# Kernel tuning notes

Measured on AMD Instinct MI355X. Metric: run time of the kernel, lower is better.

Reference implementation:

```python
import math
import jax, jax.numpy as jnp
import numpy as np

B, T, C = 2, 2048, 1024
H, Ca = 16, 64


def setup_inputs() -> dict:
    key = jax.random.key(0)
    ks = jax.random.split(key, 5)
    # kaiming-uniform-ish scale for weights
    wb = 1.0 / math.sqrt(C)
    return {
        "x": jax.random.normal(ks[0], (B, T, C), dtype=jnp.float32),
        "w_q": jax.random.uniform(ks[1], (H, C, Ca), jnp.float32, -wb, wb),
        "w_k": jax.random.uniform(ks[2], (H, C, Ca), jnp.float32, -wb, wb),
        "w_v": jax.random.uniform(ks[3], (H, C, Ca), jnp.float32, -wb, wb),
        "w_o": jax.random.uniform(ks[4], (C, C), jnp.float32, -wb, wb),
    }


def reference(x, w_q, w_k, w_v, w_o):
    # x: [B,T,C]; w_q/w_k/w_v: [H,C,Ca]; w_o: [C,C]
    scale = 1.0 / math.sqrt(w_q.shape[-1])
    q = jnp.einsum("btc,hca->bhta", x, w_q)  # [B,H,T,Ca]
    k = jnp.einsum("btc,hca->bhta", x, w_k)
    v = jnp.einsum("btc,hca->bhta", x, w_v)
    s = jnp.einsum("bhta,bhsa->bhts", q, k)  # [B,H,T,T]
    # faithful to original: mask where tril(s)==0, scale applied after masking
    s_hat = jnp.where(jnp.tril(s) == 0, -jnp.inf, s * scale)
    a = jax.nn.softmax(s_hat, axis=-1)
    y = jnp.einsum("bhts,bhsa->bhta", a, v)  # [B,H,T,Ca]
    y_cat = y.transpose(0, 2, 1, 3).reshape(x.shape)  # [B,T,C]
    return y_cat @ w_o
```

## Files before the change

kernel.cpp:

```cpp
#include <hip/hip_runtime.h>
#include <stdint.h>

#define Bc 2
#define Tc 2048
#define Cn 1024
#define Hc 16
#define CAc 64

typedef __attribute__((ext_vector_type(8))) short short8;
typedef __attribute__((ext_vector_type(4))) float f32x4;

#define QSCALE 0.18033688011112042f

__device__ __forceinline__ unsigned short f2bf(float f) {
    unsigned int u = __builtin_bit_cast(unsigned int, f);
    return (unsigned short)((u + 0x7fffu + ((u >> 16) & 1u)) >> 16);
}
__device__ __forceinline__ unsigned int pack_rne(float a, float b) {
    return (unsigned int)f2bf(a) | ((unsigned int)f2bf(b) << 16);
}
__device__ __forceinline__ unsigned int pack_trunc(float a, float b) {
    return __builtin_amdgcn_perm(__builtin_bit_cast(unsigned int, b),
                                 __builtin_bit_cast(unsigned int, a), 0x07060302u);
}

__device__ __forceinline__ void async_cp16(const unsigned short* g, unsigned short* l) {
    __builtin_amdgcn_global_load_lds(
        (const __attribute__((address_space(1))) unsigned int*)g,
        (__attribute__((address_space(3))) unsigned int*)l,
        16, 0, 0);
}

__device__ __forceinline__ int detect_bf16(const unsigned short* x) {
    int c = 0;
#pragma unroll
    for (int i = 0; i < 64; i++) {
        unsigned short u = x[i * 2];
        int e = (u >> 7) & 0xFF;
        c += (e >= 0x68 && e <= 0x90);
    }
    return c > 32;
}

__device__ __forceinline__ unsigned short ld_elem(const void* base, size_t off, int isbf) {
    return isbf ? ((const unsigned short*)base)[off] : f2bf(((const float*)base)[off]);
}

__global__ __launch_bounds__(256) void prep(
    const void* __restrict__ xin, unsigned short* __restrict__ xb,
    const void* __restrict__ wq, const void* __restrict__ wk,
    const void* __restrict__ wv, const void* __restrict__ wo,
    unsigned short* __restrict__ wT, unsigned short* __restrict__ woT)
{
    const int isbf = detect_bf16((const unsigned short*)xin);
    const int bx = blockIdx.x;
    if (bx < 4096) {
        if (isbf) return;
        int idx = (bx * 256 + threadIdx.x) * 4;
        const float* xf = (const float*)xin;
        float4 v = *(const float4*)(xf + idx);
        uint2 p;
        p.x = pack_rne(v.x, v.y);
        p.y = pack_rne(v.z, v.w);
        *(uint2*)(&xb[idx]) = p;
        return;
    }
    __shared__ unsigned short tile[32][33];
    const int t = threadIdx.x;
    const int tx = t & 31, ty = t >> 5;
    const void* src;
    unsigned short* dst;
    int R, Cw, r0, c0;
    if (bx < 7168) {
        int rem0 = bx - 4096;
        int g = rem0 >> 6;
        int rem = rem0 & 63;
        int ct = rem >> 1;
        int at = rem & 1;
        int proj = g >> 4, h = g & 15;
        const void* wsel = (proj == 0) ? wq : ((proj == 1) ? wk : wv);
        src = isbf ? (const void*)((const unsigned short*)wsel + (size_t)h * Cn * CAc)
                   : (const void*)((const float*)wsel + (size_t)h * Cn * CAc);
        dst = wT + (size_t)g * CAc * Cn;
        R = Cn; Cw = CAc; r0 = ct * 32; c0 = at * 32;
    } else {
        int rem = bx - 7168;
        src = wo; dst = woT;
        R = Cn; Cw = Cn;
        r0 = (rem >> 5) * 32; c0 = (rem & 31) * 32;
    }
#pragma unroll
    for (int j = 0; j < 4; j++)
        tile[ty + j * 8][tx] = ld_elem(src, (size_t)(r0 + ty + j * 8) * Cw + c0 + tx, isbf);
    __syncthreads();
#pragma unroll
    for (int j = 0; j < 4; j++)
        dst[(size_t)(c0 + ty + j * 8) * R + r0 + tx] = tile[tx][ty + j * 8];
}

__global__ __launch_bounds__(128, 2) void gemm_qkv(
    const void* __restrict__ xin,
    const unsigned short* __restrict__ xb,
    const unsigned short* __restrict__ Bt,
    unsigned short* __restrict__ o0,
    unsigned short* __restrict__ o1,
    unsigned short* __restrict__ o2)
{
    __shared__ alignas(16) unsigned short SH[4][128 * 32];
    const int tid = threadIdx.x;
    const int wave = tid >> 6, lane = tid & 63;
    const int l15 = lane & 15, quad = lane >> 4;
    const int mBase = blockIdx.y * 128, nBase = blockIdx.x * 128;
    const int mOff = wave * 64;

    const int isbf = detect_bf16((const unsigned short*)xin);
    const unsigned short* Amat = isbf ? (const unsigned short*)xin : xb;

    const int srow = lane >> 2;
    const int sgc  = (lane & 3) ^ (srow & 3);
    const int sw = (quad ^ (l15 & 3)) * 8;

    f32x4 acc[4][8];
#pragma unroll
    for (int i = 0; i < 4; i++)
#pragma unroll
        for (int j = 0; j < 8; j++)
            acc[i][j] = (f32x4){0.f, 0.f, 0.f, 0.f};

#pragma unroll
    for (int t = 0; t < 4; t++) {
        int rl = wave * 64 + t * 16;
        async_cp16(Amat + (size_t)(mBase + rl + srow) * Cn + sgc * 8, &SH[0][rl * 32]);
        async_cp16(Bt   + (size_t)(nBase + rl + srow) * Cn + sgc * 8, &SH[2][rl * 32]);
    }
    __syncthreads();

    for (int kk = 0; kk < 32; kk++) {
        const int cur = kk & 1;
        if (kk < 31) {
            const int k1 = (kk + 1) * 32;
#pragma unroll
            for (int t = 0; t < 4; t++) {
                int rl = wave * 64 + t * 16;
                async_cp16(Amat + (size_t)(mBase + rl + srow) * Cn + k1 + sgc * 8, &SH[1 - cur][rl * 32]);
                async_cp16(Bt   + (size_t)(nBase + rl + srow) * Cn + k1 + sgc * 8, &SH[3 - cur][rl * 32]);
            }
        }
        short8 af[4], bfr[8];
#pragma unroll
        for (int i = 0; i < 4; i++)
            af[i] = *(const short8*)(&SH[cur][(mOff + i * 16 + l15) * 32 + sw]);
#pragma unroll
        for (int j = 0; j < 8; j++)
            bfr[j] = *(const short8*)(&SH[2 + cur][(j * 16 + l15) * 32 + sw]);
#pragma unroll
        for (int i = 0; i < 4; i++)
#pragma unroll
            for (int j = 0; j < 8; j++)
                acc[i][j] = __builtin_amdgcn_mfma_f32_16x16x32_bf16(af[i], bfr[j], acc[i][j], 0, 0, 0);
        __syncthreads();
    }

    const int bb = mBase >> 11;
    if (nBase < 2048) {
        const float sc = (nBase < 1024) ? QSCALE : 1.0f;
        unsigned short* dst = (nBase < 1024) ? o0 : o1;
#pragma unroll
        for (int i = 0; i < 4; i++) {
            int m0 = mBase + mOff + i * 16 + quad * 4;
            int t0 = m0 & (Tc - 1);
#pragma unroll
            for (int j = 0; j < 8; j++) {
                int n = nBase + j * 16 + l15;
                int h = (n >> 6) & 15, a = n & 63;
                size_t base = ((size_t)(bb * Hc + h) * Tc + t0) * CAc + a;
#pragma unroll
                for (int r = 0; r < 4; r++)
                    dst[base + (size_t)r * CAc] = f2bf(acc[i][j][r] * sc);
            }
        }
    } else {
        unsigned short* Cl = &SH[0][0];
#pragma unroll
        for (int i = 0; i < 4; i++) {
            int c16 = wave * 8 + i * 2 + (quad >> 1);
            int p = quad & 1;
#pragma unroll
            for (int j = 0; j < 8; j++) {
                int nl = j * 16 + l15;
                int cs = c16 ^ (nl & 7);
                uint2 v8;
                v8.x = pack_rne(acc[i][j][0], acc[i][j][1]);
                v8.y = pack_rne(acc[i][j][2], acc[i][j][3]);
                *(uint2*)(&Cl[nl * 128 + cs * 8 + p * 4]) = v8;
            }
        }
        __syncthreads();
        const int tLoc = mBase & (Tc - 1);
#pragma unroll
        for (int pp = 0; pp < 16; pp++) {
            int vr = pp * 8 + wave * 4 + (lane >> 4);
            int cc = lane & 15;
            int cs = cc ^ (vr & 7);
            uint4 val = *(const uint4*)(&Cl[vr * 128 + cs * 8]);
            int n = nBase + vr;
            int hh = (n >> 6) & 15, a = n & 63;
            *(uint4*)(&o2[((size_t)(bb * Hc + hh) * CAc + a) * Tc + tLoc + cc * 8]) = val;
        }
    }
}

__global__ __launch_bounds__(256) void gemm_out(
    const unsigned short* __restrict__ Amat,
    const unsigned short* __restrict__ Bt,
    void* __restrict__ o0,
    const void* __restrict__ xin)
{
    __shared__ alignas(16) unsigned short Al[2][64 * 32];
    __shared__ alignas(16) unsigned short Bl[2][128 * 32];
    const int tid = threadIdx.x;
    const int wave = tid >> 6, lane = tid & 63;
    const int l15 = lane & 15, quad = lane >> 4;
    const int mBase = blockIdx.y * 64, nBase = blockIdx.x * 128;
    const int mOff = (wave & 1) * 32, nOff = (wave >> 1) * 64;

    const int isbf = detect_bf16((const unsigned short*)xin);

    const int srow = lane >> 2;
    const int sgc  = (lane & 3) ^ (srow & 3);
    const int sw = (quad ^ (l15 & 3)) * 8;

    f32x4 acc[2][4];
#pragma unroll
    for (int i = 0; i < 2; i++)
#pragma unroll
        for (int j = 0; j < 4; j++)
            acc[i][j] = (f32x4){0.f, 0.f, 0.f, 0.f};

    {
        int rlA = wave * 16;
        async_cp16(Amat + (size_t)(mBase + rlA + srow) * Cn + sgc * 8, &Al[0][rlA * 32]);
#pragma unroll
        for (int t = 0; t < 2; t++) {
            int rlB = wave * 32 + t * 16;
            async_cp16(Bt + (size_t)(nBase + rlB + srow) * Cn + sgc * 8, &Bl[0][rlB * 32]);
        }
    }
    __syncthreads();

    for (int kk = 0; kk < 32; kk++) {
        const int cur = kk & 1;
        if (kk < 31) {
            const int k1 = (kk + 1) * 32;
            int rlA = wave * 16;
            async_cp16(Amat + (size_t)(mBase + rlA + srow) * Cn + k1 + sgc * 8, &Al[1 - cur][rlA * 32]);
#pragma unroll
            for (int t = 0; t < 2; t++) {
                int rlB = wave * 32 + t * 16;
                async_cp16(Bt + (size_t)(nBase + rlB + srow) * Cn + k1 + sgc * 8, &Bl[1 - cur][rlB * 32]);
            }
        }
        short8 af[2], bfr[4];
#pragma unroll
        for (int i = 0; i < 2; i++)
            af[i] = *(const short8*)(&Al[cur][(mOff + i * 16 + l15) * 32 + sw]);
#pragma unroll
        for (int j = 0; j < 4; j++)
            bfr[j] = *(const short8*)(&Bl[cur][(nOff + j * 16 + l15) * 32 + sw]);
#pragma unroll
        for (int i = 0; i < 2; i++)
#pragma unroll
            for (int j = 0; j < 4; j++)
                acc[i][j] = __builtin_amdgcn_mfma_f32_16x16x32_bf16(af[i], bfr[j], acc[i][j], 0, 0, 0);
        __syncthreads();
    }

#pragma unroll
    for (int i = 0; i < 2; i++) {
        int m0 = mBase + mOff + i * 16 + quad * 4;
#pragma unroll
        for (int j = 0; j < 4; j++) {
            int n = nBase + nOff + j * 16 + l15;
            if (isbf) {
#pragma unroll
                for (int r = 0; r < 4; r++)
                    ((unsigned short*)o0)[(size_t)(m0 + r) * Cn + n] = f2bf(acc[i][j][r]);
            } else {
#pragma unroll
                for (int r = 0; r < 4; r++)
                    ((float*)o0)[(size_t)(m0 + r) * Cn + n] = acc[i][j][r];
            }
        }
    }
}

__global__ __launch_bounds__(256, 4) void attn_t(
    const unsigned short* __restrict__ q,
    const unsigned short* __restrict__ k,
    const unsigned short* __restrict__ vT,
    unsigned short* __restrict__ y)
{
    __shared__ alignas(16) unsigned short Kl[2][64 * 64];
    __shared__ alignas(16) unsigned short Vl[2][64 * 64];
    __shared__ alignas(16) unsigned short Pl[4][16 * 64];
    const int bx = blockIdx.x;
    const int qt = 31 - (bx >> 5);
    const int bh = bx & 31;
    const int h = bh & 15, b = bh >> 4;
    const int tid = threadIdx.x;
    const int wave = tid >> 6, lane = tid & 63;
    const int l15 = lane & 15, quad = lane >> 4;
    const int m0w = qt * 64 + wave * 16;
    const size_t bhoff = (size_t)(b * Hc + h);
    const unsigned short* qh = q + bhoff * Tc * CAc;
    const unsigned short* kh = k + bhoff * Tc * CAc;
    const unsigned short* vh = vT + bhoff * CAc * Tc;

    const int srow = (lane >> 3);
    const int sgc  = (lane & 7) ^ srow;
    const int h7 = l15 & 7;
    const int sw0 = ((quad ^ h7) << 3);
    const int sw1 = (((4 + quad) ^ h7) << 3);
    const int pw_m = 2 * h7;

    short8 qf[2];
#pragma unroll
    for (int s = 0; s < 2; s++)
        qf[s] = *(const short8*)(&qh[(size_t)(m0w + l15) * CAc + s * 32 + quad * 8]);

    f32x4 oacc[4], osum;
#pragma unroll
    for (int j2 = 0; j2 < 4; j2++) oacc[j2] = (f32x4){0.f, 0.f, 0.f, 0.f};
    osum = (f32x4){0.f, 0.f, 0.f, 0.f};

    const unsigned short ONE = 0x3F80;
    short8 ones;
#pragma unroll
    for (int i = 0; i < 8; i++) ones[i] = (short)ONE;

    unsigned short* Pw = &Pl[wave][0];

#pragma unroll
    for (int t = 0; t < 2; t++) {
        int rl = wave * 16 + t * 8;
        async_cp16(kh + (size_t)(rl + srow) * CAc + sgc * 8, &Kl[0][rl * 64]);
        async_cp16(vh + (size_t)(rl + srow) * Tc  + sgc * 8, &Vl[0][rl * 64]);
    }
    __syncthreads();

    for (int kt = 0; kt <= qt; kt++) {
        const int k0 = kt * 64;
        const int cur = kt & 1;
        if (kt < qt) {
            const unsigned short* kg = kh + (size_t)(k0 + 64) * CAc;
            const unsigned short* vg = vh + (k0 + 64);
#pragma unroll
            for (int t = 0; t < 2; t++) {
                int rl = wave * 16 + t * 8;
                async_cp16(kg + (size_t)(rl + srow) * CAc + sgc * 8, &Kl[1 - cur][rl * 64]);
                async_cp16(vg + (size_t)(rl + srow) * Tc  + sgc * 8, &Vl[1 - cur][rl * 64]);
            }
        }
        const unsigned short* Kc = Kl[cur];
        const unsigned short* Vc = Vl[cur];

        float sv[4][4];
#pragma unroll
        for (int j = 0; j < 4; j++) {
            short8 kf0 = *(const short8*)(&Kc[(j * 16 + l15) * 64 + sw0]);
            short8 kf1 = *(const short8*)(&Kc[(j * 16 + l15) * 64 + sw1]);
            f32x4 z = (f32x4){0.f, 0.f, 0.f, 0.f};
            z = __builtin_amdgcn_mfma_f32_16x16x32_bf16(kf0, qf[0], z, 0, 0, 0);
            z = __builtin_amdgcn_mfma_f32_16x16x32_bf16(kf1, qf[1], z, 0, 0, 0);
#pragma unroll
            for (int r = 0; r < 4; r++) sv[j][r] = z[r];
        }

        if (kt == qt) {
            int tg = m0w + l15;
#pragma unroll
            for (int j = 0; j < 4; j++)
#pragma unroll
                for (int r = 0; r < 4; r++) {
                    int sg = k0 + j * 16 + quad * 4 + r;
                    sv[j][r] = (sg <= tg) ? __builtin_amdgcn_exp2f(sv[j][r]) : 0.f;
                }
        } else {
#pragma unroll
            for (int j = 0; j < 4; j++)
#pragma unroll
                for (int r = 0; r < 4; r++)
                    sv[j][r] = __builtin_amdgcn_exp2f(sv[j][r]);
        }

        short8 pa[2];
#pragma unroll
        for (int j = 0; j < 4; j++) {
            uint2 v;
            v.x = pack_trunc(sv[j][0], sv[j][1]);
            v.y = pack_trunc(sv[j][2], sv[j][3]);
            *(uint2*)(&Pw[l15 * 64 + ((j * 4 + quad) ^ pw_m) * 4]) = v;
        }
#pragma unroll
        for (int c = 0; c < 2; c++)
            pa[c] = *(const short8*)(&Pw[l15 * 64 + ((c * 4 + quad) ^ h7) * 8]);

#pragma unroll
        for (int c = 0; c < 2; c++) {
#pragma unroll
            for (int j2 = 0; j2 < 4; j2++) {
                short8 vb = *(const short8*)(&Vc[(j2 * 16 + l15) * 64 + (c ? sw1 : sw0)]);
                oacc[j2] = __builtin_amdgcn_mfma_f32_16x16x32_bf16(pa[c], vb, oacc[j2], 0, 0, 0);
            }
            osum = __builtin_amdgcn_mfma_f32_16x16x32_bf16(pa[c], ones, osum, 0, 0, 0);
        }
        __syncthreads();
    }

    float ri[4];
#pragma unroll
    for (int r = 0; r < 4; r++) ri[r] = 1.0f / osum[r];
#pragma unroll
    for (int j2 = 0; j2 < 4; j2++) {
#pragma unroll
        for (int r = 0; r < 4; r++) {
            int t = m0w + quad * 4 + r;
            y[((size_t)b * Tc + t) * Cn + h * CAc + j2 * 16 + l15] = f2bf(oacc[j2][r] * ri[r]);
        }
    }
}

extern "C" void kernel_launch(void* const* d_in, const int* in_sizes, int n_in,
                              void* d_out, int out_size, void* d_ws, size_t ws_size,
                              hipStream_t stream) {
    const void* x  = d_in[0];
    const void* wq = d_in[1];
    const void* wk = d_in[2];
    const void* wv = d_in[3];
    const void* wo = d_in[4];
    char* ws = (char*)d_ws;
    unsigned short* wT  = (unsigned short*)(ws + ((size_t)1 << 20));
    unsigned short* woT = (unsigned short*)(ws + ((size_t)7 << 20));
    unsigned short* xb  = (unsigned short*)(ws + ((size_t)9 << 20));
    unsigned short* qb  = (unsigned short*)(ws + ((size_t)17 << 20));
    unsigned short* kb  = (unsigned short*)(ws + ((size_t)25 << 20));
    unsigned short* vTb = (unsigned short*)(ws + ((size_t)33 << 20));
    unsigned short* yb  = (unsigned short*)(ws + ((size_t)41 << 20));

    prep<<<dim3(8192), dim3(256), 0, stream>>>(x, xb, wq, wk, wv, wo, wT, woT);
    gemm_qkv<<<dim3(24, 32), dim3(128), 0, stream>>>(x, xb, wT, qb, kb, vTb);
    attn_t<<<dim3(1024), dim3(256), 0, stream>>>(qb, kb, vTb, yb);
    gemm_out<<<dim3(8, 64), dim3(256), 0, stream>>>(yb, woT, d_out, x);
}
```

Measured before the change: 184.9 us.

## Split attention keys across waves with register K/V and LDS reduction

Restructures the causal attention kernel so each wave handles all 64 query rows of the tile but only a 32-key slice of every 128-key block. K and V fragments are loaded straight from global memory into registers, replacing the shared-memory double buffer and the per-iteration block barrier. The partial outputs and row sums from the four waves are then combined through shared memory at the end. The change also remaps block indices across heads and lowers the occupancy hint to 2 blocks per CU, trading more registers and a final reduction for fewer barriers and less shared-memory traffic.

```diff
diff --git a/kernel.cpp b/kernel.cpp
--- a/kernel.cpp
+++ b/kernel.cpp
@@ -294,140 +294,201 @@
     }
 }
 
-__global__ __launch_bounds__(256, 4) void attn_t(
+__global__ __launch_bounds__(256, 2) void attn_t(
     const unsigned short* __restrict__ q,
     const unsigned short* __restrict__ k,
     const unsigned short* __restrict__ vT,
     unsigned short* __restrict__ y)
 {
-    __shared__ alignas(16) unsigned short Kl[2][64 * 64];
-    __shared__ alignas(16) unsigned short Vl[2][64 * 64];
-    __shared__ alignas(16) unsigned short Pl[4][16 * 64];
+    __shared__ alignas(16) float RW[4][32 * 65];
+    __shared__ float Rsum[4][64];
     const int bx = blockIdx.x;
     const int qt = 31 - (bx >> 5);
-    const int bh = bx & 31;
+    const int bh = (bx & 7) * 4 + ((bx >> 3) & 3);
     const int h = bh & 15, b = bh >> 4;
     const int tid = threadIdx.x;
     const int wave = tid >> 6, lane = tid & 63;
     const int l15 = lane & 15, quad = lane >> 4;
-    const int m0w = qt * 64 + wave * 16;
     const size_t bhoff = (size_t)(b * Hc + h);
     const unsigned short* qh = q + bhoff * Tc * CAc;
     const unsigned short* kh = k + bhoff * Tc * CAc;
     const unsigned short* vh = vT + bhoff * CAc * Tc;
 
-    const int srow = (lane >> 3);
-    const int sgc  = (lane & 7) ^ srow;
-    const int h7 = l15 & 7;
-    const int sw0 = ((quad ^ h7) << 3);
-    const int sw1 = (((4 + quad) ^ h7) << 3);
-    const int pw_m = 2 * h7;
-
-    short8 qf[2];
-#pragma unroll
-    for (int s = 0; s < 2; s++)
-        qf[s] = *(const short8*)(&qh[(size_t)(m0w + l15) * CAc + s * 32 + quad * 8]);
-
-    f32x4 oacc[4], osum;
-#pragma unroll
-    for (int j2 = 0; j2 < 4; j2++) oacc[j2] = (f32x4){0.f, 0.f, 0.f, 0.f};
-    osum = (f32x4){0.f, 0.f, 0.f, 0.f};
+    short8 qf[8];
+#pragma unroll
+    for (int qg = 0; qg < 4; qg++)
+#pragma unroll
+        for (int c = 0; c < 2; c++)
+            qf[qg * 2 + c] = *(const short8*)(
+                &qh[(size_t)(qt * 64 + qg * 16 + l15) * CAc + c * 32 + quad * 8]);
+
+    f32x4 oacc[16], osum[4];
+#pragma unroll
+    for (int i = 0; i < 16; i++) oacc[i] = (f32x4){0.f, 0.f, 0.f, 0.f};
+#pragma unroll
+    for (int i = 0; i < 4; i++) osum[i] = (f32x4){0.f, 0.f, 0.f, 0.f};
 
     const unsigned short ONE = 0x3F80;
     short8 ones;
 #pragma unroll
     for (int i = 0; i < 8; i++) ones[i] = (short)ONE;
 
-    unsigned short* Pw = &Pl[wave][0];
-
-#pragma unroll
-    for (int t = 0; t < 2; t++) {
-        int rl = wave * 16 + t * 8;
-        async_cp16(kh + (size_t)(rl + srow) * CAc + sgc * 8, &Kl[0][rl * 64]);
-        async_cp16(vh + (size_t)(rl + srow) * Tc  + sgc * 8, &Vl[0][rl * 64]);
-    }
+    unsigned short* Pw = (unsigned short*)&RW[wave][0];
+    const int hsw = l15 & 3;
+
+    const int qtmax = qt * 64 + 63;
+    const int kb_last = (qtmax >= wave * 32) ? ((qtmax - wave * 32) >> 7) : -1;
+
+    const unsigned short* kp  = kh + (size_t)(wave * 32 + l15) * CAc + quad * 8;
+    const unsigned short* vp0 = vh + (size_t)l15 * Tc + wave * 32 + quad * 8;
+    const unsigned short* vp1 = vp0 + (size_t)16 * Tc;
+    const unsigned short* vp2 = vp0 + (size_t)32 * Tc;
+    const unsigned short* vp3 = vp0 + (size_t)48 * Tc;
+
+    short8 kf[4], vbf[4];
+    if (kb_last >= 0) {
+        kf[0] = *(const short8*)(kp);
+        kf[1] = *(const short8*)(kp + 32);
+        kf[2] = *(const short8*)(kp + 16 * CAc);
+        kf[3] = *(const short8*)(kp + 16 * CAc + 32);
+        vbf[0] = *(const short8*)(vp0);
+        vbf[1] = *(const short8*)(vp1);
+        vbf[2] = *(const short8*)(vp2);
+        vbf[3] = *(const short8*)(vp3);
+    }
+
+    for (int kb = 0; kb <= kb_last; ++kb) {
+        const int k0w = kb * 128 + wave * 32;
+        const int domask = (k0w + 32 > qt * 64);
+
+        f32x4 zz[8];
+#pragma unroll
+        for (int qg = 0; qg < 4; qg++)
+#pragma unroll
+            for (int s = 0; s < 2; s++) {
+                f32x4 z = (f32x4){0.f, 0.f, 0.f, 0.f};
+                z = __builtin_amdgcn_mfma_f32_16x16x32_bf16(kf[s * 2 + 0], qf[qg * 2 + 0], z, 0, 0, 0);
+                z = __builtin_amdgcn_mfma_f32_16x16x32_bf16(kf[s * 2 + 1], qf[qg * 2 + 1], z, 0, 0, 0);
+                zz[qg * 2 + s] = z;
+            }
+
+        if (kb < kb_last) {
+            kp += 128 * CAc;
+            kf[0] = *(const short8*)(kp);
+            kf[1] = *(const short8*)(kp + 32);
+            kf[2] = *(const short8*)(kp + 16 * CAc);
+            kf[3] = *(const short8*)(kp + 16 * CAc + 32);
+        }
+
+#pragma unroll
+        for (int qg = 0; qg < 4; qg++) {
+            const int tg = qt * 64 + qg * 16 + l15;
+#pragma unroll
+            for (int s = 0; s < 2; s++) {
+                float sv[4];
+#pragma unroll
+                for (int r = 0; r < 4; r++) {
+                    float e = __builtin_amdgcn_exp2f(zz[qg * 2 + s][r]);
+                    if (domask) {
+                        int sg = k0w + s * 16 + quad * 4 + r;
+                        e = (sg <= tg) ? e : 0.f;
+                    }
+                    sv[r] = e;
+                }
+                uint2 pv;
+                pv.x = pack_trunc(sv[0], sv[1]);
+                pv.y = pack_trunc(sv[2], sv[3]);
+                *(uint2*)(&Pw[(qg * 16 + l15) * 32 +
+                              (((s * 2 + (quad >> 1)) ^ hsw) * 8) + (quad & 1) * 4]) = pv;
+            }
+        }
+
+#pragma unroll
+        for (int qg = 0; qg < 4; qg++) {
+            short8 pa = *(const short8*)(&Pw[(qg * 16 + l15) * 32 + ((quad ^ hsw) * 8)]);
+#pragma unroll
+            for (int cag = 0; cag < 4; cag++)
+                oacc[qg * 4 + cag] = __builtin_amdgcn_mfma_f32_16x16x32_bf16(pa, vbf[cag], oacc[qg * 4 + cag], 0, 0, 0);
+            osum[qg] = __builtin_amdgcn_mfma_f32_16x16x32_bf16(pa, ones, osum[qg], 0, 0, 0);
+        }
+
+        if (kb < kb_last) {
+            vp0 += 128; vp1 += 128; vp2 += 128; vp3 += 128;
+            vbf[0] = *(const short8*)(vp0);
+            vbf[1] = *(const short8*)(vp1);
+            vbf[2] = *(const short8*)(vp2);
+            vbf[3] = *(const short8*)(vp3);
+        }
+    }
+
+#pragma unroll
+    for (int qg = 0; qg < 2; qg++)
+#pragma unroll
+        for (int cag = 0; cag < 4; cag++)
+#pragma unroll
+            for (int r = 0; r < 4; r++)
+                RW[wave][(qg * 16 + quad * 4 + r) * 65 + cag * 16 + l15] = oacc[qg * 4 + cag][r];
+    if (l15 == 0)
+#pragma unroll
+        for (int qg = 0; qg < 4; qg++)
+#pragma unroll
+            for (int r = 0; r < 4; r++)
+                Rsum[wave][qg * 16 + quad * 4 + r] = osum[qg][r];
     __syncthreads();
 
-    for (int kt = 0; kt <= qt; kt++) {
-        const int k0 = kt * 64;
-        const int cur = kt & 1;
-        if (kt < qt) {
-            const unsigned short* kg = kh + (size_t)(k0 + 64) * CAc;
-            const unsigned short* vg = vh + (k0 + 64);
-#pragma unroll
-            for (int t = 0; t < 2; t++) {
-                int rl = wave * 16 + t * 8;
-                async_cp16(kg + (size_t)(rl + srow) * CAc + sgc * 8, &Kl[1 - cur][rl * 64]);
-                async_cp16(vg + (size_t)(rl + srow) * Tc  + sgc * 8, &Vl[1 - cur][rl * 64]);
-            }
-        }
-        const unsigned short* Kc = Kl[cur];
-        const unsigned short* Vc = Vl[cur];
-
-        float sv[4][4];
-#pragma unroll
-        for (int j = 0; j < 4; j++) {
-            short8 kf0 = *(const short8*)(&Kc[(j * 16 + l15) * 64 + sw0]);
-            short8 kf1 = *(const short8*)(&Kc[(j * 16 + l15) * 64 + sw1]);
-            f32x4 z = (f32x4){0.f, 0.f, 0.f, 0.f};
-            z = __builtin_amdgcn_mfma_f32_16x16x32_bf16(kf0, qf[0], z, 0, 0, 0);
-            z = __builtin_amdgcn_mfma_f32_16x16x32_bf16(kf1, qf[1], z, 0, 0, 0);
-#pragma unroll
-            for (int r = 0; r < 4; r++) sv[j][r] = z[r];
-        }
-
-        if (kt == qt) {
-            int tg = m0w + l15;
-#pragma unroll
-            for (int j = 0; j < 4; j++)
-#pragma unroll
-                for (int r = 0; r < 4; r++) {
-                    int sg = k0 + j * 16 + quad * 4 + r;
-                    sv[j][r] = (sg <= tg) ? __builtin_amdgcn_exp2f(sv[j][r]) : 0.f;
-                }
-        } else {
-#pragma unroll
-            for (int j = 0; j < 4; j++)
+    float fo[16];
+#pragma unroll
+    for (int i = 0; i < 16; i++) fo[i] = 0.f;
+    if (wave < 2) {
+#pragma unroll
+        for (int v = 0; v < 4; v++)
+#pragma unroll
+            for (int cag = 0; cag < 4; cag++)
 #pragma unroll
                 for (int r = 0; r < 4; r++)
-                    sv[j][r] = __builtin_amdgcn_exp2f(sv[j][r]);
-        }
-
-        short8 pa[2];
-#pragma unroll
-        for (int j = 0; j < 4; j++) {
-            uint2 v;
-            v.x = pack_trunc(sv[j][0], sv[j][1]);
-            v.y = pack_trunc(sv[j][2], sv[j][3]);
-            *(uint2*)(&Pw[l15 * 64 + ((j * 4 + quad) ^ pw_m) * 4]) = v;
-        }
-#pragma unroll
-        for (int c = 0; c < 2; c++)
-            pa[c] = *(const short8*)(&Pw[l15 * 64 + ((c * 4 + quad) ^ h7) * 8]);
-
-#pragma unroll
-        for (int c = 0; c < 2; c++) {
-#pragma unroll
-            for (int j2 = 0; j2 < 4; j2++) {
-                short8 vb = *(const short8*)(&Vc[(j2 * 16 + l15) * 64 + (c ? sw1 : sw0)]);
-                oacc[j2] = __builtin_amdgcn_mfma_f32_16x16x32_bf16(pa[c], vb, oacc[j2], 0, 0, 0);
-            }
-            osum = __builtin_amdgcn_mfma_f32_16x16x32_bf16(pa[c], ones, osum, 0, 0, 0);
-        }
-        __syncthreads();
-    }
-
+                    fo[cag * 4 + r] += RW[v][(wave * 16 + quad * 4 + r) * 65 + cag * 16 + l15];
+    }
+    __syncthreads();
+
+#pragma unroll
+    for (int qg = 2; qg < 4; qg++)
+#pragma unroll
+        for (int cag = 0; cag < 4; cag++)
+#pragma unroll
+            for (int r = 0; r < 4; r++)
+                RW[wave][((qg - 2) * 16 + quad * 4 + r) * 65 + cag * 16 + l15] = oacc[qg * 4 + cag][r];
+    __syncthreads();
+
+    if (wave >= 2) {
+#pragma unroll
+        for (int v = 0; v < 4; v++)
+#pragma unroll
+            for (int cag = 0; cag < 4; cag++)
+#pragma unroll
+                for (int r = 0; r < 4; r++)
+                    fo[cag * 4 + r] += RW[v][((wave - 2) * 16 + quad * 4 + r) * 65 + cag * 16 + l15];
+    }
+
+    float fs[4];
+#pragma unroll
+    for (int r = 0; r < 4; r++) {
+        float s = 0.f;
+#pragma unroll
+        for (int v = 0; v < 4; v++)
+            s += Rsum[v][wave * 16 + quad * 4 + r];
+        fs[r] = s;
+    }
     float ri[4];
 #pragma unroll
-    for (int r = 0; r < 4; r++) ri[r] = 1.0f / osum[r];
-#pragma unroll
-    for (int j2 = 0; j2 < 4; j2++) {
+    for (int r = 0; r < 4; r++) ri[r] = 1.0f / fs[r];
+
+#pragma unroll
+    for (int cag = 0; cag < 4; cag++)
 #pragma unroll
         for (int r = 0; r < 4; r++) {
-            int t = m0w + quad * 4 + r;
-            y[((size_t)b * Tc + t) * Cn + h * CAc + j2 * 16 + l15] = f2bf(oacc[j2][r] * ri[r]);
-        }
-    }
+            int t = qt * 64 + wave * 16 + quad * 4 + r;
+            y[((size_t)b * Tc + t) * Cn + h * CAc + cag * 16 + l15] = f2bf(fo[cag * 4 + r] * ri[r]);
+        }
 }
 
 extern "C" void kernel_launch(void* const* d_in, const int* in_sizes, int n_in,
```

Measured after the change: 193.9 us. 1.05x slower.
